# Kernel optimization log

Measured on AMD Instinct MI355X. Metric: run time of the kernel, lower is better.

## Reference

```python
import jax, jax.numpy as jnp
import numpy as np
import random

NQUBIT = 4
NUM_CIRCUITS = 3
SEED = 1024
C64 = jnp.complex64

SINGLE = ['rx', 'ry', 'rz', 's', 't', 'p', 'u3']
DOUBLE = ['rxx', 'ryy', 'rzz', 'swap', 'cnot', 'cp', 'ch', 'cu', 'ct', 'cz']
PCOUNT = {'rx': 1, 'ry': 1, 'rz': 1, 's': 0, 't': 0, 'p': 1, 'u3': 3,
          'rxx': 1, 'ryy': 1, 'rzz': 1, 'swap': 0, 'cnot': 0, 'cp': 1,
          'ch': 0, 'cu': 3, 'ct': 0, 'cz': 0}


def build_circuits(nqubit=NQUBIT, num_circuits=NUM_CIRCUITS, seed=SEED):
    # Replays the torch module's python `random` stream (random.seed(seed))
    rng = random.Random(seed)
    circuits, off = [], 0
    for _ in range(num_circuits):
        gates = []
        for _blk in range(3):
            for i in range(nqubit):
                g = rng.choice(SINGLE)
                gates.append((g, (i,), off, PCOUNT[g])); off += PCOUNT[g]
            c, t = rng.sample(range(0, nqubit - 1), 2)
            g = rng.choice(DOUBLE)
            gates.append((g, (c, t), off, PCOUNT[g])); off += PCOUNT[g]
        circuits.append(gates)
    return circuits, off


def u3mat(th, ph, lam):
    c = jnp.cos(th * 0.5).astype(C64)
    s = jnp.sin(th * 0.5).astype(C64)
    eip = jnp.exp(1j * ph.astype(C64))
    eil = jnp.exp(1j * lam.astype(C64))
    return jnp.stack([jnp.stack([c, -eil * s]), jnp.stack([eip * s, eip * eil * c])])


def mat1(name, p):
    if name == 's':
        return jnp.array([[1, 0], [0, 1j]], C64)
    if name == 't':
        return jnp.array([[1, 0], [0, np.exp(1j * np.pi / 4)]], C64)
    if name == 'u3':
        return u3mat(p[0], p[1], p[2])
    one = jnp.ones((), C64); zero = jnp.zeros((), C64)
    if name == 'p':
        return jnp.stack([jnp.stack([one, zero]), jnp.stack([zero, jnp.exp(1j * p[0].astype(C64))])])
    h = p[0] * 0.5
    if name == 'rx':
        c = jnp.cos(h).astype(C64); s = (-1j * jnp.sin(h)).astype(C64)
        return jnp.stack([jnp.stack([c, s]), jnp.stack([s, c])])
    if name == 'ry':
        c = jnp.cos(h).astype(C64); s = jnp.sin(h).astype(C64)
        return jnp.stack([jnp.stack([c, -s]), jnp.stack([s, c])])
    if name == 'rz':
        e = jnp.exp(-1j * h.astype(C64))
        return jnp.stack([jnp.stack([e, zero]), jnp.stack([zero, jnp.conj(e)])])
    raise ValueError(name)


def mat2(name, p):
    if name == 'swap':
        return jnp.array([[1, 0, 0, 0], [0, 0, 1, 0], [0, 1, 0, 0], [0, 0, 0, 1]], C64)
    if name == 'cnot':
        return jnp.array([[1, 0, 0, 0], [0, 1, 0, 0], [0, 0, 0, 1], [0, 0, 1, 0]], C64)
    if name == 'cz':
        return jnp.diag(jnp.array([1, 1, 1, -1], C64))
    if name == 'ct':
        return jnp.diag(jnp.array([1, 1, 1, np.exp(1j * np.pi / 4)], C64))
    if name == 'ch':
        m = np.eye(4, dtype=np.complex64); r = 1.0 / np.sqrt(2.0)
        m[2:, 2:] = [[r, r], [r, -r]]
        return jnp.asarray(m)
    if name == 'cp':
        one = jnp.ones((), C64)
        return jnp.diag(jnp.stack([one, one, one, jnp.exp(1j * p[0].astype(C64))]))
    if name == 'cu':
        return jnp.zeros((4, 4), C64).at[:2, :2].set(jnp.eye(2, dtype=C64)).at[2:, 2:].set(u3mat(p[0], p[1], p[2]))
    h = p[0] * 0.5
    if name == 'rzz':
        e = jnp.exp(-1j * h.astype(C64)); ec = jnp.conj(e)
        return jnp.diag(jnp.stack([e, ec, ec, e]))
    if name == 'rxx':
        c = jnp.cos(h).astype(C64); s = (-1j * jnp.sin(h)).astype(C64)
        XX = jnp.array([[0, 0, 0, 1], [0, 0, 1, 0], [0, 1, 0, 0], [1, 0, 0, 0]], C64)
        return c * jnp.eye(4, dtype=C64) + s * XX
    if name == 'ryy':
        c = jnp.cos(h).astype(C64); s = (1j * jnp.sin(h)).astype(C64)
        YY = jnp.array([[0, 0, 0, 1], [0, 0, -1, 0], [0, -1, 0, 0], [1, 0, 0, 0]], C64)
        return c * jnp.eye(4, dtype=C64) + s * YY
    raise ValueError(name)


def apply1(state, U, q):
    # state: (N, 2,2,2,2); contract qubit-q axis with U
    state = jnp.moveaxis(state, 1 + q, -1)
    state = state @ U.T
    return jnp.moveaxis(state, -1, 1 + q)


def apply2(state, U, q0, q1):
    state = jnp.moveaxis(state, (1 + q0, 1 + q1), (-2, -1))
    sh = state.shape
    state = (state.reshape(sh[:-2] + (4,)) @ U.T).reshape(sh)
    return jnp.moveaxis(state, (-2, -1), (1 + q0, 1 + q1))


def zsigns(nqubit):
    idx = np.arange(2 ** nqubit)
    return np.stack([1.0 - 2.0 * ((idx >> (nqubit - 1 - q)) & 1) for q in range(nqubit)]).astype(np.float32)


def run_circuit(angles, params, gates, nqubit):
    N = angles.shape[0]
    h = angles * 0.5
    # rx(angle)|0> = [cos(a/2), -i sin(a/2)] per qubit -> product state (encode layer)
    v = jnp.stack([jnp.cos(h), -1j * jnp.sin(h)], axis=-1).astype(C64)  # (N, nq, 2)
    state = jnp.ones((N,), C64)
    for i in range(nqubit):
        state = state[..., None] * v[:, i].reshape((N,) + (1,) * i + (2,))
    for (name, qs, off, cnt) in gates:
        p = params[off:off + cnt]
        if len(qs) == 1:
            state = apply1(state, mat1(name, p), qs[0])
        else:
            state = apply2(state, mat2(name, p), qs[0], qs[1])
    probs = (state.real ** 2 + state.imag ** 2).reshape(N, -1)
    return probs @ jnp.asarray(zsigns(nqubit)).T  # (N, nqubit) Pauli-Z expectations


def _forward(x, params):
    B, C, H, W = x.shape
    circuits, _ = build_circuits()
    x_unf = jnp.moveaxis(x.reshape(B, C, H // 2, 2, W), 3, 4)  # torch unfold(2, 2, 2)
    xr = x_unf.reshape(-1, NQUBIT)
    exps = [run_circuit(xr, params, g, NQUBIT) for g in circuits]
    return jnp.stack(exps, axis=1).reshape(B, NUM_CIRCUITS, W, W)


def setup_inputs():
    key = jax.random.key(0)
    k1, k2 = jax.random.split(key)
    x = jax.random.normal(k1, (512, 1, 64, 64), jnp.float32)
    _, nparams = build_circuits()
    params = jax.random.uniform(k2, (nparams,), jnp.float32, -np.pi, np.pi)
    return {"x": x, "params": params}


def reference(x, params):
    return _forward(x, params)
```

## Files before the change

kernel.cpp:

```cpp
#include <hip/hip_runtime.h>
#include <stdint.h>


namespace {

typedef _Float16 half8 __attribute__((ext_vector_type(8)));
typedef float float4v __attribute__((ext_vector_type(4)));

struct GateList {
  int ty[45];
  int q0[45];
  int q1[45];
  int off[45];
};

struct PyRandom {
  uint32_t mt[624];
  int mti;
  void init_genrand(uint32_t s) {
    mt[0] = s;
    for (int i = 1; i < 624; ++i)
      mt[i] = 1812433253u * (mt[i - 1] ^ (mt[i - 1] >> 30)) + (uint32_t)i;
    mti = 624;
  }
  void init_by_array(const uint32_t* key, int klen) {
    init_genrand(19650218u);
    int i = 1, j = 0;
    int k = 624 > klen ? 624 : klen;
    for (; k; --k) {
      mt[i] = (mt[i] ^ ((mt[i - 1] ^ (mt[i - 1] >> 30)) * 1664525u)) + key[j] + (uint32_t)j;
      ++i; ++j;
      if (i >= 624) { mt[0] = mt[623]; i = 1; }
      if (j >= klen) j = 0;
    }
    for (k = 623; k; --k) {
      mt[i] = (mt[i] ^ ((mt[i - 1] ^ (mt[i - 1] >> 30)) * 1566083941u)) - (uint32_t)i;
      ++i;
      if (i >= 624) { mt[0] = mt[623]; i = 1; }
    }
    mt[0] = 0x80000000u;
    mti = 624;
  }
  uint32_t genrand() {
    if (mti >= 624) {
      const uint32_t mag[2] = {0u, 0x9908b0dfu};
      int kk; uint32_t y;
      for (kk = 0; kk < 227; ++kk) {
        y = (mt[kk] & 0x80000000u) | (mt[kk + 1] & 0x7fffffffu);
        mt[kk] = mt[kk + 397] ^ (y >> 1) ^ mag[y & 1];
      }
      for (; kk < 623; ++kk) {
        y = (mt[kk] & 0x80000000u) | (mt[kk + 1] & 0x7fffffffu);
        mt[kk] = mt[kk - 227] ^ (y >> 1) ^ mag[y & 1];
      }
      y = (mt[623] & 0x80000000u) | (mt[0] & 0x7fffffffu);
      mt[623] = mt[396] ^ (y >> 1) ^ mag[y & 1];
      mti = 0;
    }
    uint32_t y = mt[mti++];
    y ^= y >> 11;
    y ^= (y << 7) & 0x9d2c5680u;
    y ^= (y << 15) & 0xefc60000u;
    y ^= y >> 18;
    return y;
  }
  uint32_t getrandbits(int k) { return genrand() >> (32 - k); }
  uint32_t randbelow(uint32_t n) {
    int k = 32 - __builtin_clz(n);
    uint32_t r = getrandbits(k);
    while (r >= n) r = getrandbits(k);
    return r;
  }
};

void build_gatelist(GateList& gl) {
  PyRandom rng;
  uint32_t key = 1024u;
  rng.init_by_array(&key, 1);
  static const int PC_S[7]  = {1, 1, 1, 0, 0, 1, 3};
  static const int PC_D[10] = {1, 1, 1, 0, 0, 1, 0, 3, 0, 0};
  int off = 0, idx = 0;
  for (int circ = 0; circ < 3; ++circ) {
    for (int blk = 0; blk < 3; ++blk) {
      for (int i = 0; i < 4; ++i) {
        int g = (int)rng.randbelow(7);
        gl.ty[idx] = g; gl.q0[idx] = i; gl.q1[idx] = 0; gl.off[idx] = off;
        off += PC_S[g]; ++idx;
      }
      int pool[3] = {0, 1, 2};
      int j0 = (int)rng.randbelow(3); int c = pool[j0]; pool[j0] = pool[2];
      int j1 = (int)rng.randbelow(2); int t = pool[j1];
      int g = (int)rng.randbelow(10);
      gl.ty[idx] = 10 + g; gl.q0[idx] = c; gl.q1[idx] = t; gl.off[idx] = off;
      off += PC_D[g]; ++idx;
    }
  }
}

__device__ inline float2 cmul(float2 a, float2 b) {
  return make_float2(a.x * b.x - a.y * b.y, a.x * b.y + a.y * b.x);
}
__device__ inline float2 cadd(float2 a, float2 b) {
  return make_float2(a.x + b.x, a.y + b.y);
}
__device__ inline float2 shflx(float2 v, int m) {
  return make_float2(__shfl_xor(v.x, m), __shfl_xor(v.y, m));
}

__global__ __launch_bounds__(768) void build_unitaries(
    const float* __restrict__ params, _Float16* __restrict__ Uws, GateList gl) {
  int tid = threadIdx.x;
  if (tid >= 768) return;
  int circ = tid >> 8;
  int col  = (tid >> 4) & 15;
  int k    = tid & 15;

  float2 s = make_float2(k == col ? 1.f : 0.f, 0.f);

  for (int g = 0; g < 15; ++g) {
    int gi = circ * 15 + g;
    int ty = gl.ty[gi];
    int o  = gl.off[gi];
    if (ty < 7) {
      float2 G00 = make_float2(1, 0), G01 = make_float2(0, 0),
             G10 = make_float2(0, 0), G11 = make_float2(1, 0);
      if (ty == 0) {
        float c, sn; __sincosf(params[o] * 0.5f, &sn, &c);
        G00 = make_float2(c, 0); G01 = make_float2(0, -sn);
        G10 = make_float2(0, -sn); G11 = make_float2(c, 0);
      } else if (ty == 1) {
        float c, sn; __sincosf(params[o] * 0.5f, &sn, &c);
        G00 = make_float2(c, 0); G01 = make_float2(-sn, 0);
        G10 = make_float2(sn, 0); G11 = make_float2(c, 0);
      } else if (ty == 2) {
        float c, sn; __sincosf(params[o] * 0.5f, &sn, &c);
        G00 = make_float2(c, -sn); G11 = make_float2(c, sn);
      } else if (ty == 3) {
        G11 = make_float2(0, 1);
      } else if (ty == 4) {
        G11 = make_float2(0.7071067811865476f, 0.7071067811865476f);
      } else if (ty == 5) {
        float cp, sp; __sincosf(params[o], &sp, &cp);
        G11 = make_float2(cp, sp);
      } else {
        float th = params[o], phv = params[o + 1], lm = params[o + 2];
        float c, sn; __sincosf(th * 0.5f, &sn, &c);
        float cp, sp; __sincosf(phv, &sp, &cp);
        float cl, sl; __sincosf(lm, &sl, &cl);
        G00 = make_float2(c, 0);
        G01 = make_float2(-cl * sn, -sl * sn);
        G10 = make_float2(cp * sn, sp * sn);
        G11 = make_float2((cp * cl - sp * sl) * c, (cp * sl + sp * cl) * c);
      }
      int m = 1 << (3 - gl.q0[gi]);
      bool hib = (k & m) != 0;
      float2 p = shflx(s, m);
      float2 A = hib ? G11 : G00;
      float2 B = hib ? G10 : G01;
      s = cadd(cmul(A, s), cmul(B, p));
    } else {
      float2 G[4][4];
#pragma unroll
      for (int r2 = 0; r2 < 4; ++r2)
#pragma unroll
        for (int c2 = 0; c2 < 4; ++c2) G[r2][c2] = make_float2(0, 0);
      if (ty == 10) {
        float c, sn; __sincosf(params[o] * 0.5f, &sn, &c);
        G[0][0] = G[1][1] = G[2][2] = G[3][3] = make_float2(c, 0);
        G[0][3] = G[1][2] = G[2][1] = G[3][0] = make_float2(0, -sn);
      } else if (ty == 11) {
        float c, sn; __sincosf(params[o] * 0.5f, &sn, &c);
        G[0][0] = G[1][1] = G[2][2] = G[3][3] = make_float2(c, 0);
        G[0][3] = G[3][0] = make_float2(0, sn);
        G[1][2] = G[2][1] = make_float2(0, -sn);
      } else if (ty == 12) {
        float c, sn; __sincosf(params[o] * 0.5f, &sn, &c);
        G[0][0] = G[3][3] = make_float2(c, -sn);
        G[1][1] = G[2][2] = make_float2(c, sn);
      } else if (ty == 13) {
        G[0][0] = make_float2(1, 0); G[1][2] = make_float2(1, 0);
        G[2][1] = make_float2(1, 0); G[3][3] = make_float2(1, 0);
      } else if (ty == 14) {
        G[0][0] = G[1][1] = make_float2(1, 0);
        G[2][3] = G[3][2] = make_float2(1, 0);
      } else if (ty == 15) {
        G[0][0] = G[1][1] = G[2][2] = make_float2(1, 0);
        float cp, sp; __sincosf(params[o], &sp, &cp);
        G[3][3] = make_float2(cp, sp);
      } else if (ty == 16) {
        G[0][0] = G[1][1] = make_float2(1, 0);
        float rv = 0.7071067811865476f;
        G[2][2] = make_float2(rv, 0); G[2][3] = make_float2(rv, 0);
        G[3][2] = make_float2(rv, 0); G[3][3] = make_float2(-rv, 0);
      } else if (ty == 17) {
        G[0][0] = G[1][1] = make_float2(1, 0);
        float th = params[o], phv = params[o + 1], lm = params[o + 2];
        float c, sn; __sincosf(th * 0.5f, &sn, &c);
        float cp, sp; __sincosf(phv, &sp, &cp);
        float cl, sl; __sincosf(lm, &sl, &cl);
        G[2][2] = make_float2(c, 0);
        G[2][3] = make_float2(-cl * sn, -sl * sn);
        G[3][2] = make_float2(cp * sn, sp * sn);
        G[3][3] = make_float2((cp * cl - sp * sl) * c, (cp * sl + sp * cl) * c);
      } else if (ty == 18) {
        G[0][0] = G[1][1] = G[2][2] = make_float2(1, 0);
        G[3][3] = make_float2(0.7071067811865476f, 0.7071067811865476f);
      } else {
        G[0][0] = G[1][1] = G[2][2] = make_float2(1, 0);
        G[3][3] = make_float2(-1, 0);
      }
      int m0 = 1 << (3 - gl.q0[gi]);
      int m1 = 1 << (3 - gl.q1[gi]);
      bool b0 = (k & m0) != 0;
      bool b1 = (k & m1) != 0;
      float2 p0 = s;
      float2 p1 = shflx(s, m1);
      float2 p2 = shflx(s, m0);
      float2 p3 = shflx(s, m0 ^ m1);
      float2 acc = make_float2(0, 0);
#pragma unroll
      for (int j = 0; j < 4; ++j) {
        float2 r0 = b1 ? G[1][1 ^ j] : G[0][0 ^ j];
        float2 r1 = b1 ? G[3][3 ^ j] : G[2][2 ^ j];
        float2 coef = b0 ? r1 : r0;
        float2 pj = (j == 0) ? p0 : (j == 1) ? p1 : (j == 2) ? p2 : p3;
        acc = cadd(acc, cmul(coef, pj));
      }
      s = acc;
    }
  }

  int pc = __popc(col) & 3;
  float2 ph = make_float2(1, 0);
  if (pc == 1) ph = make_float2(0, -1);
  else if (pc == 2) ph = make_float2(-1, 0);
  else if (pc == 3) ph = make_float2(0, 1);
  float2 v = cmul(s, ph);

  int L = ((col >> 3) << 4) | k;
  int j = col & 7;
  Uws[((2 * circ) * 32 + L) * 8 + j]     = (_Float16)v.x;
  Uws[((2 * circ + 1) * 32 + L) * 8 + j] = (_Float16)v.y;
}

__global__ __launch_bounds__(256) void qconv_main(
    const float* __restrict__ x, const _Float16* __restrict__ Ufrag,
    float* __restrict__ out) {
  __shared__ _Float16 lds[256 * 24];
  const int tid  = threadIdx.x;
  const int wid  = tid >> 6;
  const int lane = tid & 63;
  const int quad = lane >> 4;
  const int n16  = lane & 15;
  const int rowbase = blockIdx.x * 256 + wid * 64;
  const int r = rowbase + lane;

  half8 af[6];
  if (lane < 32) {
    const half8* Uv = (const half8*)Ufrag;
#pragma unroll
    for (int bb = 0; bb < 6; ++bb) af[bb] = Uv[bb * 32 + lane];
  } else {
#pragma unroll
    for (int bb = 0; bb < 6; ++bb)
#pragma unroll
      for (int e = 0; e < 8; ++e) af[bb][e] = (_Float16)0.f;
  }

  const int b  = r >> 10;
  const int h2 = (r >> 5) & 31;
  const int j  = r & 31;
  const float* xb = x + b * 4096 + h2 * 128 + j * 2;
  float2 lo = *(const float2*)(xb);
  float2 hi = *(const float2*)(xb + 64);
  float c0, s0, c1, s1, c2, s2, c3, s3;
  __sincosf(lo.x * 0.5f, &s0, &c0);
  __sincosf(hi.x * 0.5f, &s1, &c1);
  __sincosf(lo.y * 0.5f, &s2, &c2);
  __sincosf(hi.y * 0.5f, &s3, &c3);
  float t01[4] = {c0 * c1, c0 * s1, s0 * c1, s0 * s1};
  float t23[4] = {c2 * c3, c2 * s3, s2 * c3, s2 * s3};
  __align__(16) _Float16 rh[16];
#pragma unroll
  for (int a = 0; a < 4; ++a)
#pragma unroll
    for (int bq = 0; bq < 4; ++bq)
      rh[a * 4 + bq] = (_Float16)(t01[a] * t23[bq]);

  half8* dst = (half8*)&lds[tid * 24];
  dst[0] = *(const half8*)&rh[0];
  dst[1] = *(const half8*)&rh[8];
  __syncthreads();

#pragma unroll
  for (int t = 0; t < 4; ++t) {
    half8 bf;
    if (quad < 2) {
      bf = *(const half8*)&lds[(wid * 64 + t * 16 + n16) * 24 + quad * 8];
    } else {
#pragma unroll
      for (int e = 0; e < 8; ++e) bf[e] = (_Float16)0.f;
    }
    float4v acc[6];
#pragma unroll
    for (int bb = 0; bb < 6; ++bb) {
      float4v z = {0.f, 0.f, 0.f, 0.f};
      acc[bb] = __builtin_amdgcn_mfma_f32_16x16x32_f16(af[bb], bf, z, 0, 0, 0);
    }
    float4 E[3];
#pragma unroll
    for (int c = 0; c < 3; ++c) {
      float pv[4];
#pragma unroll
      for (int v = 0; v < 4; ++v) {
        float re = acc[2 * c][v], im = acc[2 * c + 1][v];
        pv[v] = fmaf(re, re, im * im);
      }
      float sA = pv[0] + pv[1], dA = pv[0] - pv[1];
      float sB = pv[2] + pv[3], dB = pv[2] - pv[3];
      float A00 = sA + sB;
      float A01 = dA + dB;
      float A10 = sA - sB;
      float r3 = A01 + __shfl_xor(A01, 16); r3 += __shfl_xor(r3, 32);
      float r2 = A10 + __shfl_xor(A10, 16); r2 += __shfl_xor(r2, 32);
      float h16v = __shfl_xor(A00, 16);
      float Ssum = A00 + h16v;
      float Dv = (quad & 1) ? (h16v - A00) : (A00 - h16v);
      float r1 = Dv + __shfl_xor(Dv, 32);
      float S32 = __shfl_xor(Ssum, 32);
      float r0 = (quad & 2) ? (S32 - Ssum) : (Ssum - S32);
      E[c] = make_float4(r0, r1, r2, r3);
    }
    if (quad < 3) {
      float4 ev = (quad == 0) ? E[0] : (quad == 1 ? E[1] : E[2]);
      int rowg = rowbase + t * 16 + n16;
      *(float4*)(out + (size_t)rowg * 12 + quad * 4) = ev;
    }
  }
}

}

extern "C" void kernel_launch(void* const* d_in, const int* in_sizes, int n_in,
                              void* d_out, int out_size, void* d_ws, size_t ws_size,
                              hipStream_t stream) {
  const float* x      = (const float*)d_in[0];
  const float* params = (const float*)d_in[1];
  float* out = (float*)d_out;
  _Float16* Uws = (_Float16*)d_ws;

  GateList gl;
  build_gatelist(gl);

  hipLaunchKernelGGL(build_unitaries, dim3(1), dim3(768), 0, stream,
                     params, Uws, gl);

  int nrows = in_sizes[0] / 4;
  int grid  = nrows / 256;
  hipLaunchKernelGGL(qconv_main, dim3(grid), dim3(256), 0, stream,
                     x, Uws, out);
}
```

Measured before the change: 91.55 us.

## Fuse unitary construction into main kernel and enlarge blocks to 1024 threads

Removes the separate single-block kernel that built the circuit unitaries into workspace, and recomputes them in shared memory at the start of every block of the main kernel. Blocks grow from 256 to 1024 threads so the redundant build is spread over more rows. This removes a launch and the serial dependency between the two kernels. In exchange every block repeats the gate-building work, and the larger shared-memory footprint may limit occupancy.

After: 92.84 us. About the same (+1.4%).

```diff
diff --git a/kernel.cpp b/kernel.cpp
--- a/kernel.cpp
+++ b/kernel.cpp
@@ -107,165 +107,19 @@
   return make_float2(__shfl_xor(v.x, m), __shfl_xor(v.y, m));
 }
 
-__global__ __launch_bounds__(768) void build_unitaries(
-    const float* __restrict__ params, _Float16* __restrict__ Uws, GateList gl) {
-  int tid = threadIdx.x;
-  if (tid >= 768) return;
-  int circ = tid >> 8;
-  int col  = (tid >> 4) & 15;
-  int k    = tid & 15;
-
-  float2 s = make_float2(k == col ? 1.f : 0.f, 0.f);
-
-  for (int g = 0; g < 15; ++g) {
-    int gi = circ * 15 + g;
-    int ty = gl.ty[gi];
-    int o  = gl.off[gi];
-    if (ty < 7) {
-      float2 G00 = make_float2(1, 0), G01 = make_float2(0, 0),
-             G10 = make_float2(0, 0), G11 = make_float2(1, 0);
-      if (ty == 0) {
-        float c, sn; __sincosf(params[o] * 0.5f, &sn, &c);
-        G00 = make_float2(c, 0); G01 = make_float2(0, -sn);
-        G10 = make_float2(0, -sn); G11 = make_float2(c, 0);
-      } else if (ty == 1) {
-        float c, sn; __sincosf(params[o] * 0.5f, &sn, &c);
-        G00 = make_float2(c, 0); G01 = make_float2(-sn, 0);
-        G10 = make_float2(sn, 0); G11 = make_float2(c, 0);
-      } else if (ty == 2) {
-        float c, sn; __sincosf(params[o] * 0.5f, &sn, &c);
-        G00 = make_float2(c, -sn); G11 = make_float2(c, sn);
-      } else if (ty == 3) {
-        G11 = make_float2(0, 1);
-      } else if (ty == 4) {
-        G11 = make_float2(0.7071067811865476f, 0.7071067811865476f);
-      } else if (ty == 5) {
-        float cp, sp; __sincosf(params[o], &sp, &cp);
-        G11 = make_float2(cp, sp);
-      } else {
-        float th = params[o], phv = params[o + 1], lm = params[o + 2];
-        float c, sn; __sincosf(th * 0.5f, &sn, &c);
-        float cp, sp; __sincosf(phv, &sp, &cp);
-        float cl, sl; __sincosf(lm, &sl, &cl);
-        G00 = make_float2(c, 0);
-        G01 = make_float2(-cl * sn, -sl * sn);
-        G10 = make_float2(cp * sn, sp * sn);
-        G11 = make_float2((cp * cl - sp * sl) * c, (cp * sl + sp * cl) * c);
-      }
-      int m = 1 << (3 - gl.q0[gi]);
-      bool hib = (k & m) != 0;
-      float2 p = shflx(s, m);
-      float2 A = hib ? G11 : G00;
-      float2 B = hib ? G10 : G01;
-      s = cadd(cmul(A, s), cmul(B, p));
-    } else {
-      float2 G[4][4];
-#pragma unroll
-      for (int r2 = 0; r2 < 4; ++r2)
-#pragma unroll
-        for (int c2 = 0; c2 < 4; ++c2) G[r2][c2] = make_float2(0, 0);
-      if (ty == 10) {
-        float c, sn; __sincosf(params[o] * 0.5f, &sn, &c);
-        G[0][0] = G[1][1] = G[2][2] = G[3][3] = make_float2(c, 0);
-        G[0][3] = G[1][2] = G[2][1] = G[3][0] = make_float2(0, -sn);
-      } else if (ty == 11) {
-        float c, sn; __sincosf(params[o] * 0.5f, &sn, &c);
-        G[0][0] = G[1][1] = G[2][2] = G[3][3] = make_float2(c, 0);
-        G[0][3] = G[3][0] = make_float2(0, sn);
-        G[1][2] = G[2][1] = make_float2(0, -sn);
-      } else if (ty == 12) {
-        float c, sn; __sincosf(params[o] * 0.5f, &sn, &c);
-        G[0][0] = G[3][3] = make_float2(c, -sn);
-        G[1][1] = G[2][2] = make_float2(c, sn);
-      } else if (ty == 13) {
-        G[0][0] = make_float2(1, 0); G[1][2] = make_float2(1, 0);
-        G[2][1] = make_float2(1, 0); G[3][3] = make_float2(1, 0);
-      } else if (ty == 14) {
-        G[0][0] = G[1][1] = make_float2(1, 0);
-        G[2][3] = G[3][2] = make_float2(1, 0);
-      } else if (ty == 15) {
-        G[0][0] = G[1][1] = G[2][2] = make_float2(1, 0);
-        float cp, sp; __sincosf(params[o], &sp, &cp);
-        G[3][3] = make_float2(cp, sp);
-      } else if (ty == 16) {
-        G[0][0] = G[1][1] = make_float2(1, 0);
-        float rv = 0.7071067811865476f;
-        G[2][2] = make_float2(rv, 0); G[2][3] = make_float2(rv, 0);
-        G[3][2] = make_float2(rv, 0); G[3][3] = make_float2(-rv, 0);
-      } else if (ty == 17) {
-        G[0][0] = G[1][1] = make_float2(1, 0);
-        float th = params[o], phv = params[o + 1], lm = params[o + 2];
-        float c, sn; __sincosf(th * 0.5f, &sn, &c);
-        float cp, sp; __sincosf(phv, &sp, &cp);
-        float cl, sl; __sincosf(lm, &sl, &cl);
-        G[2][2] = make_float2(c, 0);
-        G[2][3] = make_float2(-cl * sn, -sl * sn);
-        G[3][2] = make_float2(cp * sn, sp * sn);
-        G[3][3] = make_float2((cp * cl - sp * sl) * c, (cp * sl + sp * cl) * c);
-      } else if (ty == 18) {
-        G[0][0] = G[1][1] = G[2][2] = make_float2(1, 0);
-        G[3][3] = make_float2(0.7071067811865476f, 0.7071067811865476f);
-      } else {
-        G[0][0] = G[1][1] = G[2][2] = make_float2(1, 0);
-        G[3][3] = make_float2(-1, 0);
-      }
-      int m0 = 1 << (3 - gl.q0[gi]);
-      int m1 = 1 << (3 - gl.q1[gi]);
-      bool b0 = (k & m0) != 0;
-      bool b1 = (k & m1) != 0;
-      float2 p0 = s;
-      float2 p1 = shflx(s, m1);
-      float2 p2 = shflx(s, m0);
-      float2 p3 = shflx(s, m0 ^ m1);
-      float2 acc = make_float2(0, 0);
-#pragma unroll
-      for (int j = 0; j < 4; ++j) {
-        float2 r0 = b1 ? G[1][1 ^ j] : G[0][0 ^ j];
-        float2 r1 = b1 ? G[3][3 ^ j] : G[2][2 ^ j];
-        float2 coef = b0 ? r1 : r0;
-        float2 pj = (j == 0) ? p0 : (j == 1) ? p1 : (j == 2) ? p2 : p3;
-        acc = cadd(acc, cmul(coef, pj));
-      }
-      s = acc;
-    }
-  }
-
-  int pc = __popc(col) & 3;
-  float2 ph = make_float2(1, 0);
-  if (pc == 1) ph = make_float2(0, -1);
-  else if (pc == 2) ph = make_float2(-1, 0);
-  else if (pc == 3) ph = make_float2(0, 1);
-  float2 v = cmul(s, ph);
-
-  int L = ((col >> 3) << 4) | k;
-  int j = col & 7;
-  Uws[((2 * circ) * 32 + L) * 8 + j]     = (_Float16)v.x;
-  Uws[((2 * circ + 1) * 32 + L) * 8 + j] = (_Float16)v.y;
-}
-
-__global__ __launch_bounds__(256) void qconv_main(
-    const float* __restrict__ x, const _Float16* __restrict__ Ufrag,
-    float* __restrict__ out) {
-  __shared__ _Float16 lds[256 * 24];
+__global__ __launch_bounds__(1024, 4) void qconv_fused(
+    const float* __restrict__ x, const float* __restrict__ params,
+    float* __restrict__ out, GateList gl) {
+  __shared__ _Float16 ufrag[1536];
+  __shared__ _Float16 lds[1024 * 24];
+
   const int tid  = threadIdx.x;
   const int wid  = tid >> 6;
   const int lane = tid & 63;
   const int quad = lane >> 4;
   const int n16  = lane & 15;
-  const int rowbase = blockIdx.x * 256 + wid * 64;
+  const int rowbase = blockIdx.x * 1024 + wid * 64;
   const int r = rowbase + lane;
-
-  half8 af[6];
-  if (lane < 32) {
-    const half8* Uv = (const half8*)Ufrag;
-#pragma unroll
-    for (int bb = 0; bb < 6; ++bb) af[bb] = Uv[bb * 32 + lane];
-  } else {
-#pragma unroll
-    for (int bb = 0; bb < 6; ++bb)
-#pragma unroll
-      for (int e = 0; e < 8; ++e) af[bb][e] = (_Float16)0.f;
-  }
 
   const int b  = r >> 10;
   const int h2 = (r >> 5) & 31;
@@ -273,6 +127,140 @@
   const float* xb = x + b * 4096 + h2 * 128 + j * 2;
   float2 lo = *(const float2*)(xb);
   float2 hi = *(const float2*)(xb + 64);
+
+  if (tid < 768) {
+    const int circ = tid >> 8;
+    const int col  = (tid >> 4) & 15;
+    const int k    = tid & 15;
+
+    float2 s = make_float2(k == col ? 1.f : 0.f, 0.f);
+
+    for (int g = 0; g < 15; ++g) {
+      int gi = circ * 15 + g;
+      int ty = gl.ty[gi];
+      int o  = gl.off[gi];
+      if (ty < 7) {
+        float2 G00 = make_float2(1, 0), G01 = make_float2(0, 0),
+               G10 = make_float2(0, 0), G11 = make_float2(1, 0);
+        if (ty == 0) {
+          float c, sn; __sincosf(params[o] * 0.5f, &sn, &c);
+          G00 = make_float2(c, 0); G01 = make_float2(0, -sn);
+          G10 = make_float2(0, -sn); G11 = make_float2(c, 0);
+        } else if (ty == 1) {
+          float c, sn; __sincosf(params[o] * 0.5f, &sn, &c);
+          G00 = make_float2(c, 0); G01 = make_float2(-sn, 0);
+          G10 = make_float2(sn, 0); G11 = make_float2(c, 0);
+        } else if (ty == 2) {
+          float c, sn; __sincosf(params[o] * 0.5f, &sn, &c);
+          G00 = make_float2(c, -sn); G11 = make_float2(c, sn);
+        } else if (ty == 3) {
+          G11 = make_float2(0, 1);
+        } else if (ty == 4) {
+          G11 = make_float2(0.7071067811865476f, 0.7071067811865476f);
+        } else if (ty == 5) {
+          float cp, sp; __sincosf(params[o], &sp, &cp);
+          G11 = make_float2(cp, sp);
+        } else {
+          float th = params[o], phv = params[o + 1], lm = params[o + 2];
+          float c, sn; __sincosf(th * 0.5f, &sn, &c);
+          float cp, sp; __sincosf(phv, &sp, &cp);
+          float cl, sl; __sincosf(lm, &sl, &cl);
+          G00 = make_float2(c, 0);
+          G01 = make_float2(-cl * sn, -sl * sn);
+          G10 = make_float2(cp * sn, sp * sn);
+          G11 = make_float2((cp * cl - sp * sl) * c, (cp * sl + sp * cl) * c);
+        }
+        int m = 1 << (3 - gl.q0[gi]);
+        bool hib = (k & m) != 0;
+        float2 p = shflx(s, m);
+        float2 A = hib ? G11 : G00;
+        float2 B = hib ? G10 : G01;
+        s = cadd(cmul(A, s), cmul(B, p));
+      } else {
+        float2 G[4][4];
+#pragma unroll
+        for (int r2 = 0; r2 < 4; ++r2)
+#pragma unroll
+          for (int c2 = 0; c2 < 4; ++c2) G[r2][c2] = make_float2(0, 0);
+        if (ty == 10) {
+          float c, sn; __sincosf(params[o] * 0.5f, &sn, &c);
+          G[0][0] = G[1][1] = G[2][2] = G[3][3] = make_float2(c, 0);
+          G[0][3] = G[1][2] = G[2][1] = G[3][0] = make_float2(0, -sn);
+        } else if (ty == 11) {
+          float c, sn; __sincosf(params[o] * 0.5f, &sn, &c);
+          G[0][0] = G[1][1] = G[2][2] = G[3][3] = make_float2(c, 0);
+          G[0][3] = G[3][0] = make_float2(0, sn);
+          G[1][2] = G[2][1] = make_float2(0, -sn);
+        } else if (ty == 12) {
+          float c, sn; __sincosf(params[o] * 0.5f, &sn, &c);
+          G[0][0] = G[3][3] = make_float2(c, -sn);
+          G[1][1] = G[2][2] = make_float2(c, sn);
+        } else if (ty == 13) {
+          G[0][0] = make_float2(1, 0); G[1][2] = make_float2(1, 0);
+          G[2][1] = make_float2(1, 0); G[3][3] = make_float2(1, 0);
+        } else if (ty == 14) {
+          G[0][0] = G[1][1] = make_float2(1, 0);
+          G[2][3] = G[3][2] = make_float2(1, 0);
+        } else if (ty == 15) {
+          G[0][0] = G[1][1] = G[2][2] = make_float2(1, 0);
+          float cp, sp; __sincosf(params[o], &sp, &cp);
+          G[3][3] = make_float2(cp, sp);
+        } else if (ty == 16) {
+          G[0][0] = G[1][1] = make_float2(1, 0);
+          float rv = 0.7071067811865476f;
+          G[2][2] = make_float2(rv, 0); G[2][3] = make_float2(rv, 0);
+          G[3][2] = make_float2(rv, 0); G[3][3] = make_float2(-rv, 0);
+        } else if (ty == 17) {
+          G[0][0] = G[1][1] = make_float2(1, 0);
+          float th = params[o], phv = params[o + 1], lm = params[o + 2];
+          float c, sn; __sincosf(th * 0.5f, &sn, &c);
+          float cp, sp; __sincosf(phv, &sp, &cp);
+          float cl, sl; __sincosf(lm, &sl, &cl);
+          G[2][2] = make_float2(c, 0);
+          G[2][3] = make_float2(-cl * sn, -sl * sn);
+          G[3][2] = make_float2(cp * sn, sp * sn);
+          G[3][3] = make_float2((cp * cl - sp * sl) * c, (cp * sl + sp * cl) * c);
+        } else if (ty == 18) {
+          G[0][0] = G[1][1] = G[2][2] = make_float2(1, 0);
+          G[3][3] = make_float2(0.7071067811865476f, 0.7071067811865476f);
+        } else {
+          G[0][0] = G[1][1] = G[2][2] = make_float2(1, 0);
+          G[3][3] = make_float2(-1, 0);
+        }
+        int m0 = 1 << (3 - gl.q0[gi]);
+        int m1 = 1 << (3 - gl.q1[gi]);
+        bool b0 = (k & m0) != 0;
+        bool b1 = (k & m1) != 0;
+        float2 p0 = s;
+        float2 p1 = shflx(s, m1);
+        float2 p2 = shflx(s, m0);
+        float2 p3 = shflx(s, m0 ^ m1);
+        float2 acc = make_float2(0, 0);
+#pragma unroll
+        for (int jj = 0; jj < 4; ++jj) {
+          float2 r0 = b1 ? G[1][1 ^ jj] : G[0][0 ^ jj];
+          float2 r1 = b1 ? G[3][3 ^ jj] : G[2][2 ^ jj];
+          float2 coef = b0 ? r1 : r0;
+          float2 pj = (jj == 0) ? p0 : (jj == 1) ? p1 : (jj == 2) ? p2 : p3;
+          acc = cadd(acc, cmul(coef, pj));
+        }
+        s = acc;
+      }
+    }
+
+    int pc = __popc(col) & 3;
+    float2 ph = make_float2(1, 0);
+    if (pc == 1) ph = make_float2(0, -1);
+    else if (pc == 2) ph = make_float2(-1, 0);
+    else if (pc == 3) ph = make_float2(0, 1);
+    float2 v = cmul(s, ph);
+
+    int L = ((col >> 3) << 4) | k;
+    int jf = col & 7;
+    ufrag[((2 * circ) * 32 + L) * 8 + jf]     = (_Float16)v.x;
+    ufrag[((2 * circ + 1) * 32 + L) * 8 + jf] = (_Float16)v.y;
+  }
+
   float c0, s0, c1, s1, c2, s2, c3, s3;
   __sincosf(lo.x * 0.5f, &s0, &c0);
   __sincosf(hi.x * 0.5f, &s1, &c1);
@@ -290,7 +278,20 @@
   half8* dst = (half8*)&lds[tid * 24];
   dst[0] = *(const half8*)&rh[0];
   dst[1] = *(const half8*)&rh[8];
+
   __syncthreads();
+
+  half8 af[6];
+  if (lane < 32) {
+    const half8* Uv = (const half8*)ufrag;
+#pragma unroll
+    for (int bb = 0; bb < 6; ++bb) af[bb] = Uv[bb * 32 + lane];
+  } else {
+#pragma unroll
+    for (int bb = 0; bb < 6; ++bb)
+#pragma unroll
+      for (int e = 0; e < 8; ++e) af[bb][e] = (_Float16)0.f;
+  }
 
 #pragma unroll
   for (int t = 0; t < 4; ++t) {
@@ -347,16 +348,13 @@
   const float* x      = (const float*)d_in[0];
   const float* params = (const float*)d_in[1];
   float* out = (float*)d_out;
-  _Float16* Uws = (_Float16*)d_ws;
+  (void)d_ws; (void)ws_size;
 
   GateList gl;
   build_gatelist(gl);
 
-  hipLaunchKernelGGL(build_unitaries, dim3(1), dim3(768), 0, stream,
-                     params, Uws, gl);
-
   int nrows = in_sizes[0] / 4;
-  int grid  = nrows / 256;
-  hipLaunchKernelGGL(qconv_main, dim3(grid), dim3(256), 0, stream,
-                     x, Uws, out);
-}
+  int grid  = nrows / 1024;
+  hipLaunchKernelGGL(qconv_fused, dim3(grid), dim3(1024), 0, stream,
+                     x, params, out, gl);
+}
```
